# Performance work log

Measured on AMD Instinct MI355X. Metric: run time of the kernel, lower is better.

Reference implementation:

```python
import jax, jax.numpy as jnp
import numpy as np

FEATURE_DIM, HIDDEN_DIM, ATTN_DIM = 2048, 1024, 1024
B, L = 128, 196


def setup_inputs() -> dict:
    key = jax.random.key(0)
    ks = jax.random.split(key, 8)
    s_enc = 1.0 / np.sqrt(FEATURE_DIM)
    s_hid = 1.0 / np.sqrt(HIDDEN_DIM)
    s_full = 1.0 / np.sqrt(ATTN_DIM)
    return {
        "encoder_out": jax.random.normal(ks[0], (B, L, FEATURE_DIM), jnp.float32),
        "hidden": jax.random.normal(ks[1], (B, HIDDEN_DIM), jnp.float32),
        "W_enc": jax.random.uniform(ks[2], (FEATURE_DIM, ATTN_DIM), jnp.float32, -s_enc, s_enc),
        "b_enc": jax.random.uniform(ks[3], (ATTN_DIM,), jnp.float32, -s_enc, s_enc),
        "W_hid": jax.random.uniform(ks[4], (HIDDEN_DIM, ATTN_DIM), jnp.float32, -s_hid, s_hid),
        "b_hid": jax.random.uniform(ks[5], (ATTN_DIM,), jnp.float32, -s_hid, s_hid),
        "W_full": jax.random.uniform(ks[6], (ATTN_DIM,), jnp.float32, -s_full, s_full),
        "b_full": jax.random.uniform(ks[7], (1,), jnp.float32, -s_full, s_full),
    }


def reference(encoder_out, hidden, W_enc, b_enc, W_hid, b_hid, W_full, b_full):
    # attn1: (B, L, A)
    attn1 = jnp.einsum("blf,fa->bla", encoder_out, W_enc) + b_enc
    # attn2: (B, 1, A)
    attn2 = (hidden @ W_hid + b_hid)[:, None, :]
    attn = jax.nn.relu(attn1 + attn2)
    # scalar score per location: (B, L)
    scores = jnp.einsum("bla,a->bl", attn, W_full) + b_full[0]
    alpha = jax.nn.softmax(scores, axis=1)
    # weighted sum over L: (B, F)
    context = jnp.einsum("blf,bl->bf", encoder_out, alpha)
    return context, alpha
```

## Files before the change

### kernel.cpp

```cpp
#include <hip/hip_runtime.h>
#include <hip/hip_bf16.h>

typedef unsigned short u16;
typedef short s16x8 __attribute__((ext_vector_type(8)));
typedef float f32x4 __attribute__((ext_vector_type(4)));

#define F_DIM 2048
#define A_DIM 1024
#define H_DIM 1024
#define BATCH 128
#define LLEN  196
#define MROWS (BATCH * LLEN)
#define LDA   40

__device__ __forceinline__ u16 f2b(float x) {
  union { float f; unsigned int u; } c; c.f = x;
  unsigned int r = (c.u + 0x7fffu + ((c.u >> 16) & 1u)) >> 16;
  return (u16)r;
}

__device__ __forceinline__ void gload_lds16(const void* g, void* l) {
  __builtin_amdgcn_global_load_lds((const __attribute__((address_space(1))) void*)g,
                                   (__attribute__((address_space(3))) void*)l, 16, 0, 0);
}

__global__ void wenc_cvt_kernel(const float* __restrict__ W, u16* __restrict__ WT) {
  __shared__ float tile[32][33];
  int kb = blockIdx.x * 32, ab = blockIdx.y * 32;
  int t = threadIdx.x;
  int r = t >> 3, c = (t & 7) * 4;
  float4 v = *(const float4*)&W[(size_t)(kb + r) * A_DIM + ab + c];
  tile[r][c] = v.x; tile[r][c + 1] = v.y; tile[r][c + 2] = v.z; tile[r][c + 3] = v.w;
  __syncthreads();
  ushort4 o;
  o.x = f2b(tile[c + 0][r]);
  o.y = f2b(tile[c + 1][r]);
  o.z = f2b(tile[c + 2][r]);
  o.w = f2b(tile[c + 3][r]);
  *(ushort4*)&WT[(size_t)(ab + r) * F_DIM + kb + c] = o;
}

__global__ void enc_cvt_kernel(const float* __restrict__ enc, u16* __restrict__ encb) {
  int idx = blockIdx.x * 256 + threadIdx.x;
  const float4* src = (const float4*)enc;
  uint4* dst = (uint4*)encb;
  #pragma unroll
  for (int it = 0; it < 8; ++it) {
    size_t p = (size_t)idx + (size_t)it * 802816;
    float4 v0 = src[p * 2], v1 = src[p * 2 + 1];
    union { u16 u[8]; uint4 q; } o;
    o.u[0] = f2b(v0.x); o.u[1] = f2b(v0.y); o.u[2] = f2b(v0.z); o.u[3] = f2b(v0.w);
    o.u[4] = f2b(v1.x); o.u[5] = f2b(v1.y); o.u[6] = f2b(v1.z); o.u[7] = f2b(v1.w);
    dst[p] = o.q;
  }
}

__global__ void attn2_kernel(const float* __restrict__ hidden, const float* __restrict__ W_hid,
                             const float* __restrict__ b_hid, const float* __restrict__ b_enc,
                             float* __restrict__ attn2p) {
  __shared__ float hl[8][256];
  int t = threadIdx.x;
  int a  = blockIdx.x * 256 + t;
  int b0 = blockIdx.y * 8;
  int k0 = blockIdx.z * 256;
  {
    int j = t >> 5, kk = (t & 31) * 8;
    float4 v0 = *(const float4*)&hidden[(size_t)(b0 + j) * H_DIM + k0 + kk];
    float4 v1 = *(const float4*)&hidden[(size_t)(b0 + j) * H_DIM + k0 + kk + 4];
    hl[j][kk + 0] = v0.x; hl[j][kk + 1] = v0.y; hl[j][kk + 2] = v0.z; hl[j][kk + 3] = v0.w;
    hl[j][kk + 4] = v1.x; hl[j][kk + 5] = v1.y; hl[j][kk + 6] = v1.z; hl[j][kk + 7] = v1.w;
  }
  __syncthreads();
  float acc[8] = {0.f, 0.f, 0.f, 0.f, 0.f, 0.f, 0.f, 0.f};
  #pragma unroll 4
  for (int k = 0; k < 256; ++k) {
    float w = W_hid[(size_t)(k0 + k) * A_DIM + a];
    #pragma unroll
    for (int j = 0; j < 8; ++j) acc[j] = fmaf(hl[j][k], w, acc[j]);
  }
  if (blockIdx.z == 0) {
    float bias = b_hid[a] + b_enc[a];
    #pragma unroll
    for (int j = 0; j < 8; ++j) acc[j] += bias;
  }
  #pragma unroll
  for (int j = 0; j < 8; ++j) atomicAdd(&attn2p[(size_t)(b0 + j) * A_DIM + a], acc[j]);
}

__global__ void gemm_score_bf16(const u16* __restrict__ encb, const u16* __restrict__ WT,
                                const float* __restrict__ attn2p, const float* __restrict__ W_full,
                                float* __restrict__ scores) {
  __shared__ __align__(16) u16 As[128 * 32];
  __shared__ __align__(16) u16 Bs[128 * 32];
  __shared__ float wf_lds[128];
  __shared__ float at2_lds[2][128];

  int n0 = blockIdx.x * 128;
  int m0 = blockIdx.y * 128;
  int t = threadIdx.x;

  int b0 = m0 / LLEN;
  int bnd = (b0 + 1) * LLEN;
  int b1 = min(b0 + 1, BATCH - 1);

  if (t < 128) {
    wf_lds[t] = W_full[n0 + t];
    at2_lds[0][t] = attn2p[(size_t)b0 * A_DIM + n0 + t];
    at2_lds[1][t] = attn2p[(size_t)b1 * A_DIM + n0 + t];
  }

  int lane = t & 63, wave = t >> 6;
  int wr = wave >> 1, wc = wave & 1;
  int c16 = lane & 15, quad = lane >> 4;

  f32x4 acc[4][4];
  #pragma unroll
  for (int i = 0; i < 4; ++i)
    #pragma unroll
    for (int j = 0; j < 4; ++j) acc[i][j] = (f32x4){0.f, 0.f, 0.f, 0.f};

  const u16* agp0 = encb + (size_t)(m0 + (t >> 2)) * F_DIM + (t & 3) * 8;
  const u16* agp1 = agp0 + (size_t)64 * F_DIM;
  const u16* bgp0 = WT + (size_t)(n0 + (t >> 2)) * F_DIM + (t & 3) * 8;
  const u16* bgp1 = bgp0 + (size_t)64 * F_DIM;
  u16* al = As + wave * 512;
  u16* bl = Bs + wave * 512;

  for (int kt = 0; kt < F_DIM; kt += 32) {
    gload_lds16(agp0 + kt, al);
    gload_lds16(agp1 + kt, al + 2048);
    gload_lds16(bgp0 + kt, bl);
    gload_lds16(bgp1 + kt, bl + 2048);
    __syncthreads();
    s16x8 af[4], bf[4];
    #pragma unroll
    for (int i = 0; i < 4; ++i) {
      af[i] = *(const s16x8*)&As[(wr * 64 + i * 16 + c16) * 32 + quad * 8];
      bf[i] = *(const s16x8*)&Bs[(wc * 64 + i * 16 + c16) * 32 + quad * 8];
    }
    #pragma unroll
    for (int mi = 0; mi < 4; ++mi)
      #pragma unroll
      for (int ni = 0; ni < 4; ++ni)
        acc[mi][ni] = __builtin_amdgcn_mfma_f32_16x16x32_bf16(af[mi], bf[ni], acc[mi][ni], 0, 0, 0);
    __syncthreads();
  }

  float wf[4], a2a[4], a2b[4];
  #pragma unroll
  for (int ni = 0; ni < 4; ++ni) {
    int col = wc * 64 + ni * 16 + c16;
    wf[ni] = wf_lds[col];
    a2a[ni] = at2_lds[0][col];
    a2b[ni] = at2_lds[1][col];
  }
  #pragma unroll
  for (int mi = 0; mi < 4; ++mi) {
    #pragma unroll
    for (int r = 0; r < 4; ++r) {
      int row_g = m0 + wr * 64 + mi * 16 + quad * 4 + r;
      bool hi = row_g >= bnd;
      float p = 0.f;
      #pragma unroll
      for (int ni = 0; ni < 4; ++ni) {
        float v = acc[mi][ni][r] + (hi ? a2b[ni] : a2a[ni]);
        v = fmaxf(v, 0.f);
        p = fmaf(v, wf[ni], p);
      }
      p += __shfl_xor(p, 1);
      p += __shfl_xor(p, 2);
      p += __shfl_xor(p, 4);
      p += __shfl_xor(p, 8);
      if (c16 == 0) atomicAdd(&scores[row_g], p);
    }
  }
}

__global__ void gemm_score_f32(const float* __restrict__ enc, const u16* __restrict__ WT,
                               const float* __restrict__ attn2p, const float* __restrict__ W_full,
                               float* __restrict__ scores) {
  __shared__ __align__(16) u16 As[128 * LDA];
  __shared__ __align__(16) u16 Bs[128 * LDA];
  __shared__ float wf_lds[128];
  __shared__ float at2_lds[2][128];

  int n0 = blockIdx.x * 128;
  int m0 = blockIdx.y * 128;
  int t = threadIdx.x;
  int b0 = m0 / LLEN;
  int bnd = (b0 + 1) * LLEN;
  int b1 = min(b0 + 1, BATCH - 1);
  if (t < 128) {
    wf_lds[t] = W_full[n0 + t];
    at2_lds[0][t] = attn2p[(size_t)b0 * A_DIM + n0 + t];
    at2_lds[1][t] = attn2p[(size_t)b1 * A_DIM + n0 + t];
  }
  int lane = t & 63, wave = t >> 6;
  int wr = wave >> 1, wc = wave & 1;
  int c16 = lane & 15, quad = lane >> 4;
  f32x4 acc[4][4];
  #pragma unroll
  for (int i = 0; i < 4; ++i)
    #pragma unroll
    for (int j = 0; j < 4; ++j) acc[i][j] = (f32x4){0.f, 0.f, 0.f, 0.f};
  int ar = t >> 3, ac = (t & 7) * 4;
  int br = t >> 2, bc = (t & 3) * 8;
  const float* ap = enc + (size_t)(m0 + ar) * F_DIM + ac;
  const u16*  bp = WT + (size_t)(n0 + br) * F_DIM + bc;
  for (int kt = 0; kt < F_DIM; kt += 32) {
    #pragma unroll
    for (int p = 0; p < 4; ++p) {
      float4 v = *(const float4*)(ap + (size_t)p * 32 * F_DIM + kt);
      ushort4 u;
      u.x = f2b(v.x); u.y = f2b(v.y); u.z = f2b(v.z); u.w = f2b(v.w);
      *(ushort4*)&As[(ar + p * 32) * LDA + ac] = u;
    }
    #pragma unroll
    for (int p = 0; p < 2; ++p) {
      uint4 v = *(const uint4*)(bp + (size_t)p * 64 * F_DIM + kt);
      *(uint4*)&Bs[(br + p * 64) * LDA + bc] = v;
    }
    __syncthreads();
    s16x8 af[4], bf[4];
    #pragma unroll
    for (int i = 0; i < 4; ++i) {
      af[i] = *(const s16x8*)&As[(wr * 64 + i * 16 + c16) * LDA + quad * 8];
      bf[i] = *(const s16x8*)&Bs[(wc * 64 + i * 16 + c16) * LDA + quad * 8];
    }
    #pragma unroll
    for (int mi = 0; mi < 4; ++mi)
      #pragma unroll
      for (int ni = 0; ni < 4; ++ni)
        acc[mi][ni] = __builtin_amdgcn_mfma_f32_16x16x32_bf16(af[mi], bf[ni], acc[mi][ni], 0, 0, 0);
    __syncthreads();
  }
  float wf[4], a2a[4], a2b[4];
  #pragma unroll
  for (int ni = 0; ni < 4; ++ni) {
    int col = wc * 64 + ni * 16 + c16;
    wf[ni] = wf_lds[col];
    a2a[ni] = at2_lds[0][col];
    a2b[ni] = at2_lds[1][col];
  }
  #pragma unroll
  for (int mi = 0; mi < 4; ++mi) {
    #pragma unroll
    for (int r = 0; r < 4; ++r) {
      int row_g = m0 + wr * 64 + mi * 16 + quad * 4 + r;
      bool hi = row_g >= bnd;
      float p = 0.f;
      #pragma unroll
      for (int ni = 0; ni < 4; ++ni) {
        float v = acc[mi][ni][r] + (hi ? a2b[ni] : a2a[ni]);
        v = fmaxf(v, 0.f);
        p = fmaf(v, wf[ni], p);
      }
      p += __shfl_xor(p, 1);
      p += __shfl_xor(p, 2);
      p += __shfl_xor(p, 4);
      p += __shfl_xor(p, 8);
      if (c16 == 0) atomicAdd(&scores[row_g], p);
    }
  }
}

__global__ void softmax_kernel(const float* __restrict__ scores, float* __restrict__ alpha) {
  __shared__ float red[8];
  int b = blockIdx.x, t = threadIdx.x;
  float s = (t < LLEN) ? scores[b * LLEN + t] : -3.0e38f;
  float m = s;
  #pragma unroll
  for (int o = 1; o <= 32; o <<= 1) m = fmaxf(m, __shfl_xor(m, o));
  if ((t & 63) == 0) red[t >> 6] = m;
  __syncthreads();
  m = fmaxf(fmaxf(red[0], red[1]), fmaxf(red[2], red[3]));
  float e = (t < LLEN) ? expf(s - m) : 0.f;
  float sum = e;
  #pragma unroll
  for (int o = 1; o <= 32; o <<= 1) sum += __shfl_xor(sum, o);
  __syncthreads();
  if ((t & 63) == 0) red[4 + (t >> 6)] = sum;
  __syncthreads();
  sum = red[4] + red[5] + red[6] + red[7];
  if (t < LLEN) alpha[b * LLEN + t] = e / sum;
}

__global__ void context_kernel(const float* __restrict__ enc, const float* __restrict__ alpha,
                               float* __restrict__ out) {
  __shared__ float al[49];
  int b = blockIdx.y, t = threadIdx.x;
  int l0 = blockIdx.z * 49;
  int f4 = blockIdx.x * 256 + t;
  if (t < 49) al[t] = alpha[b * LLEN + l0 + t];
  __syncthreads();
  const float4* e4 = (const float4*)enc + ((size_t)b * LLEN + l0) * (F_DIM / 4) + f4;
  float4 acc = {0.f, 0.f, 0.f, 0.f};
  #pragma unroll 7
  for (int l = 0; l < 49; ++l) {
    float4 v = e4[(size_t)l * (F_DIM / 4)];
    float a = al[l];
    acc.x = fmaf(v.x, a, acc.x);
    acc.y = fmaf(v.y, a, acc.y);
    acc.z = fmaf(v.z, a, acc.z);
    acc.w = fmaf(v.w, a, acc.w);
  }
  float* o = out + (size_t)b * F_DIM + f4 * 4;
  atomicAdd(o + 0, acc.x);
  atomicAdd(o + 1, acc.y);
  atomicAdd(o + 2, acc.z);
  atomicAdd(o + 3, acc.w);
}

extern "C" void kernel_launch(void* const* d_in, const int* in_sizes, int n_in,
                              void* d_out, int out_size, void* d_ws, size_t ws_size,
                              hipStream_t stream) {
  const float* enc    = (const float*)d_in[0];
  const float* hidden = (const float*)d_in[1];
  const float* W_enc  = (const float*)d_in[2];
  const float* b_enc  = (const float*)d_in[3];
  const float* W_hid  = (const float*)d_in[4];
  const float* b_hid  = (const float*)d_in[5];
  const float* W_full = (const float*)d_in[6];
  float* out = (float*)d_out;
  float* alpha_out = out + (size_t)BATCH * F_DIM;

  const size_t encb_bytes = (size_t)MROWS * F_DIM * sizeof(u16);
  const size_t wt_bytes   = (size_t)A_DIM * F_DIM * sizeof(u16);
  const size_t a2_bytes   = (size_t)BATCH * A_DIM * sizeof(float);
  const size_t sc_bytes   = (size_t)MROWS * sizeof(float);
  char* ws = (char*)d_ws;

  if (ws_size >= encb_bytes + wt_bytes + a2_bytes + sc_bytes) {
    u16*   encb   = (u16*)ws;
    u16*   WT     = (u16*)(ws + encb_bytes);
    float* attn2p = (float*)(ws + encb_bytes + wt_bytes);
    float* scores = (float*)(ws + encb_bytes + wt_bytes + a2_bytes);

    hipMemsetAsync(attn2p, 0, a2_bytes, stream);
    hipMemsetAsync(scores, 0, sc_bytes, stream);
    hipMemsetAsync(out, 0, (size_t)BATCH * F_DIM * sizeof(float), stream);

    wenc_cvt_kernel<<<dim3(F_DIM / 32, A_DIM / 32), 256, 0, stream>>>(W_enc, WT);
    enc_cvt_kernel<<<dim3(3136), 256, 0, stream>>>(enc, encb);
    attn2_kernel<<<dim3(A_DIM / 256, BATCH / 8, 4), 256, 0, stream>>>(hidden, W_hid, b_hid, b_enc, attn2p);
    gemm_score_bf16<<<dim3(A_DIM / 128, MROWS / 128), 256, 0, stream>>>(encb, WT, attn2p, W_full, scores);
    softmax_kernel<<<dim3(BATCH), 256, 0, stream>>>(scores, alpha_out);
    context_kernel<<<dim3(F_DIM / 4 / 256, BATCH, 4), 256, 0, stream>>>(enc, alpha_out, out);
  } else {
    u16*   WT     = (u16*)ws;
    float* attn2p = (float*)(ws + wt_bytes);
    float* scores = (float*)(ws + wt_bytes + a2_bytes);

    hipMemsetAsync(attn2p, 0, a2_bytes, stream);
    hipMemsetAsync(scores, 0, sc_bytes, stream);
    hipMemsetAsync(out, 0, (size_t)BATCH * F_DIM * sizeof(float), stream);

    wenc_cvt_kernel<<<dim3(F_DIM / 32, A_DIM / 32), 256, 0, stream>>>(W_enc, WT);
    attn2_kernel<<<dim3(A_DIM / 256, BATCH / 8, 4), 256, 0, stream>>>(hidden, W_hid, b_hid, b_enc, attn2p);
    gemm_score_f32<<<dim3(A_DIM / 128, MROWS / 128), 256, 0, stream>>>(enc, WT, attn2p, W_full, scores);
    softmax_kernel<<<dim3(BATCH), 256, 0, stream>>>(scores, alpha_out);
    context_kernel<<<dim3(F_DIM / 4 / 256, BATCH, 4), 256, 0, stream>>>(enc, alpha_out, out);
  }
}
```

Baseline: 534.4 us.

## Swizzle GEMM tile order for L2 reuse and compute context from bf16 encoder

The bf16 GEMM now runs on a 1D grid remapped so that groups of 8 M-tiles sweep all N-tiles together, which is meant to keep A and B tiles resident in L2 and cut DRAM re-reads. The context reduction now reads the bf16 copy of the encoder output instead of the fp32 original, halving the bytes streamed. That kernel uses fewer, larger blocks with 28 rows each. The cost is reduced precision in the context output, since encoder values are bf16-rounded, and more atomics into the output.

```diff
diff --git a/kernel.cpp b/kernel.cpp
--- a/kernel.cpp
+++ b/kernel.cpp
@@ -17,6 +17,11 @@
   union { float f; unsigned int u; } c; c.f = x;
   unsigned int r = (c.u + 0x7fffu + ((c.u >> 16) & 1u)) >> 16;
   return (u16)r;
+}
+
+__device__ __forceinline__ float b2f(u16 x) {
+  union { unsigned int u; float f; } c; c.u = ((unsigned int)x) << 16;
+  return c.f;
 }
 
 __device__ __forceinline__ void gload_lds16(const void* g, void* l) {
@@ -95,8 +100,16 @@
   __shared__ float wf_lds[128];
   __shared__ float at2_lds[2][128];
 
-  int n0 = blockIdx.x * 128;
-  int m0 = blockIdx.y * 128;
+  int i = blockIdx.x;
+  int g  = i >> 6;
+  int r  = i & 63;
+  int y  = r >> 3;
+  int gi = r & 7;
+  int mt = g * 8 + gi;
+  if (mt >= MROWS / 128) return;
+
+  int n0 = y * 128;
+  int m0 = mt * 128;
   int t = threadIdx.x;
 
   int b0 = m0 / LLEN;
@@ -115,9 +128,9 @@
 
   f32x4 acc[4][4];
   #pragma unroll
-  for (int i = 0; i < 4; ++i)
-    #pragma unroll
-    for (int j = 0; j < 4; ++j) acc[i][j] = (f32x4){0.f, 0.f, 0.f, 0.f};
+  for (int ii = 0; ii < 4; ++ii)
+    #pragma unroll
+    for (int j = 0; j < 4; ++j) acc[ii][j] = (f32x4){0.f, 0.f, 0.f, 0.f};
 
   const u16* agp0 = encb + (size_t)(m0 + (t >> 2)) * F_DIM + (t & 3) * 8;
   const u16* agp1 = agp0 + (size_t)64 * F_DIM;
@@ -134,9 +147,9 @@
     __syncthreads();
     s16x8 af[4], bf[4];
     #pragma unroll
-    for (int i = 0; i < 4; ++i) {
-      af[i] = *(const s16x8*)&As[(wr * 64 + i * 16 + c16) * 32 + quad * 8];
-      bf[i] = *(const s16x8*)&Bs[(wc * 64 + i * 16 + c16) * 32 + quad * 8];
+    for (int ii = 0; ii < 4; ++ii) {
+      af[ii] = *(const s16x8*)&As[(wr * 64 + ii * 16 + c16) * 32 + quad * 8];
+      bf[ii] = *(const s16x8*)&Bs[(wc * 64 + ii * 16 + c16) * 32 + quad * 8];
     }
     #pragma unroll
     for (int mi = 0; mi < 4; ++mi)
@@ -146,6 +159,94 @@
     __syncthreads();
   }
 
+  float wf[4], a2a[4], a2b[4];
+  #pragma unroll
+  for (int ni = 0; ni < 4; ++ni) {
+    int col = wc * 64 + ni * 16 + c16;
+    wf[ni] = wf_lds[col];
+    a2a[ni] = at2_lds[0][col];
+    a2b[ni] = at2_lds[1][col];
+  }
+  #pragma unroll
+  for (int mi = 0; mi < 4; ++mi) {
+    #pragma unroll
+    for (int rr = 0; rr < 4; ++rr) {
+      int row_g = m0 + wr * 64 + mi * 16 + quad * 4 + rr;
+      bool hi = row_g >= bnd;
+      float p = 0.f;
+      #pragma unroll
+      for (int ni = 0; ni < 4; ++ni) {
+        float v = acc[mi][ni][rr] + (hi ? a2b[ni] : a2a[ni]);
+        v = fmaxf(v, 0.f);
+        p = fmaf(v, wf[ni], p);
+      }
+      p += __shfl_xor(p, 1);
+      p += __shfl_xor(p, 2);
+      p += __shfl_xor(p, 4);
+      p += __shfl_xor(p, 8);
+      if (c16 == 0) atomicAdd(&scores[row_g], p);
+    }
+  }
+}
+
+__global__ void gemm_score_f32(const float* __restrict__ enc, const u16* __restrict__ WT,
+                               const float* __restrict__ attn2p, const float* __restrict__ W_full,
+                               float* __restrict__ scores) {
+  __shared__ __align__(16) u16 As[128 * LDA];
+  __shared__ __align__(16) u16 Bs[128 * LDA];
+  __shared__ float wf_lds[128];
+  __shared__ float at2_lds[2][128];
+
+  int n0 = blockIdx.x * 128;
+  int m0 = blockIdx.y * 128;
+  int t = threadIdx.x;
+  int b0 = m0 / LLEN;
+  int bnd = (b0 + 1) * LLEN;
+  int b1 = min(b0 + 1, BATCH - 1);
+  if (t < 128) {
+    wf_lds[t] = W_full[n0 + t];
+    at2_lds[0][t] = attn2p[(size_t)b0 * A_DIM + n0 + t];
+    at2_lds[1][t] = attn2p[(size_t)b1 * A_DIM + n0 + t];
+  }
+  int lane = t & 63, wave = t >> 6;
+  int wr = wave >> 1, wc = wave & 1;
+  int c16 = lane & 15, quad = lane >> 4;
+  f32x4 acc[4][4];
+  #pragma unroll
+  for (int i = 0; i < 4; ++i)
+    #pragma unroll
+    for (int j = 0; j < 4; ++j) acc[i][j] = (f32x4){0.f, 0.f, 0.f, 0.f};
+  int ar = t >> 3, ac = (t & 7) * 4;
+  int br = t >> 2, bc = (t & 3) * 8;
+  const float* ap = enc + (size_t)(m0 + ar) * F_DIM + ac;
+  const u16*  bp = WT + (size_t)(n0 + br) * F_DIM + bc;
+  for (int kt = 0; kt < F_DIM; kt += 32) {
+    #pragma unroll
+    for (int p = 0; p < 4; ++p) {
+      float4 v = *(const float4*)(ap + (size_t)p * 32 * F_DIM + kt);
+      ushort4 u;
+      u.x = f2b(v.x); u.y = f2b(v.y); u.z = f2b(v.z); u.w = f2b(v.w);
+      *(ushort4*)&As[(ar + p * 32) * LDA + ac] = u;
+    }
+    #pragma unroll
+    for (int p = 0; p < 2; ++p) {
+      uint4 v = *(const uint4*)(bp + (size_t)p * 64 * F_DIM + kt);
+      *(uint4*)&Bs[(br + p * 64) * LDA + bc] = v;
+    }
+    __syncthreads();
+    s16x8 af[4], bf[4];
+    #pragma unroll
+    for (int i = 0; i < 4; ++i) {
+      af[i] = *(const s16x8*)&As[(wr * 64 + i * 16 + c16) * LDA + quad * 8];
+      bf[i] = *(const s16x8*)&Bs[(wc * 64 + i * 16 + c16) * LDA + quad * 8];
+    }
+    #pragma unroll
+    for (int mi = 0; mi < 4; ++mi)
+      #pragma unroll
+      for (int ni = 0; ni < 4; ++ni)
+        acc[mi][ni] = __builtin_amdgcn_mfma_f32_16x16x32_bf16(af[mi], bf[ni], acc[mi][ni], 0, 0, 0);
+    __syncthreads();
+  }
   float wf[4], a2a[4], a2b[4];
   #pragma unroll
   for (int ni = 0; ni < 4; ++ni) {
@@ -176,94 +277,6 @@
   }
 }
 
-__global__ void gemm_score_f32(const float* __restrict__ enc, const u16* __restrict__ WT,
-                               const float* __restrict__ attn2p, const float* __restrict__ W_full,
-                               float* __restrict__ scores) {
-  __shared__ __align__(16) u16 As[128 * LDA];
-  __shared__ __align__(16) u16 Bs[128 * LDA];
-  __shared__ float wf_lds[128];
-  __shared__ float at2_lds[2][128];
-
-  int n0 = blockIdx.x * 128;
-  int m0 = blockIdx.y * 128;
-  int t = threadIdx.x;
-  int b0 = m0 / LLEN;
-  int bnd = (b0 + 1) * LLEN;
-  int b1 = min(b0 + 1, BATCH - 1);
-  if (t < 128) {
-    wf_lds[t] = W_full[n0 + t];
-    at2_lds[0][t] = attn2p[(size_t)b0 * A_DIM + n0 + t];
-    at2_lds[1][t] = attn2p[(size_t)b1 * A_DIM + n0 + t];
-  }
-  int lane = t & 63, wave = t >> 6;
-  int wr = wave >> 1, wc = wave & 1;
-  int c16 = lane & 15, quad = lane >> 4;
-  f32x4 acc[4][4];
-  #pragma unroll
-  for (int i = 0; i < 4; ++i)
-    #pragma unroll
-    for (int j = 0; j < 4; ++j) acc[i][j] = (f32x4){0.f, 0.f, 0.f, 0.f};
-  int ar = t >> 3, ac = (t & 7) * 4;
-  int br = t >> 2, bc = (t & 3) * 8;
-  const float* ap = enc + (size_t)(m0 + ar) * F_DIM + ac;
-  const u16*  bp = WT + (size_t)(n0 + br) * F_DIM + bc;
-  for (int kt = 0; kt < F_DIM; kt += 32) {
-    #pragma unroll
-    for (int p = 0; p < 4; ++p) {
-      float4 v = *(const float4*)(ap + (size_t)p * 32 * F_DIM + kt);
-      ushort4 u;
-      u.x = f2b(v.x); u.y = f2b(v.y); u.z = f2b(v.z); u.w = f2b(v.w);
-      *(ushort4*)&As[(ar + p * 32) * LDA + ac] = u;
-    }
-    #pragma unroll
-    for (int p = 0; p < 2; ++p) {
-      uint4 v = *(const uint4*)(bp + (size_t)p * 64 * F_DIM + kt);
-      *(uint4*)&Bs[(br + p * 64) * LDA + bc] = v;
-    }
-    __syncthreads();
-    s16x8 af[4], bf[4];
-    #pragma unroll
-    for (int i = 0; i < 4; ++i) {
-      af[i] = *(const s16x8*)&As[(wr * 64 + i * 16 + c16) * LDA + quad * 8];
-      bf[i] = *(const s16x8*)&Bs[(wc * 64 + i * 16 + c16) * LDA + quad * 8];
-    }
-    #pragma unroll
-    for (int mi = 0; mi < 4; ++mi)
-      #pragma unroll
-      for (int ni = 0; ni < 4; ++ni)
-        acc[mi][ni] = __builtin_amdgcn_mfma_f32_16x16x32_bf16(af[mi], bf[ni], acc[mi][ni], 0, 0, 0);
-    __syncthreads();
-  }
-  float wf[4], a2a[4], a2b[4];
-  #pragma unroll
-  for (int ni = 0; ni < 4; ++ni) {
-    int col = wc * 64 + ni * 16 + c16;
-    wf[ni] = wf_lds[col];
-    a2a[ni] = at2_lds[0][col];
-    a2b[ni] = at2_lds[1][col];
-  }
-  #pragma unroll
-  for (int mi = 0; mi < 4; ++mi) {
-    #pragma unroll
-    for (int r = 0; r < 4; ++r) {
-      int row_g = m0 + wr * 64 + mi * 16 + quad * 4 + r;
-      bool hi = row_g >= bnd;
-      float p = 0.f;
-      #pragma unroll
-      for (int ni = 0; ni < 4; ++ni) {
-        float v = acc[mi][ni][r] + (hi ? a2b[ni] : a2a[ni]);
-        v = fmaxf(v, 0.f);
-        p = fmaf(v, wf[ni], p);
-      }
-      p += __shfl_xor(p, 1);
-      p += __shfl_xor(p, 2);
-      p += __shfl_xor(p, 4);
-      p += __shfl_xor(p, 8);
-      if (c16 == 0) atomicAdd(&scores[row_g], p);
-    }
-  }
-}
-
 __global__ void softmax_kernel(const float* __restrict__ scores, float* __restrict__ alpha) {
   __shared__ float red[8];
   int b = blockIdx.x, t = threadIdx.x;
@@ -283,6 +296,28 @@
   __syncthreads();
   sum = red[4] + red[5] + red[6] + red[7];
   if (t < LLEN) alpha[b * LLEN + t] = e / sum;
+}
+
+__global__ void context_bf16_kernel(const u16* __restrict__ encb, const float* __restrict__ alpha,
+                                    float* __restrict__ out) {
+  __shared__ float al[28];
+  int b = blockIdx.y, t = threadIdx.x;
+  int l0 = blockIdx.x * 28;
+  if (t < 28) al[t] = alpha[b * LLEN + l0 + t];
+  __syncthreads();
+  const uint4* e4 = (const uint4*)(encb + ((size_t)b * LLEN + l0) * F_DIM) + t;
+  float acc[8] = {0.f, 0.f, 0.f, 0.f, 0.f, 0.f, 0.f, 0.f};
+  #pragma unroll 4
+  for (int l = 0; l < 28; ++l) {
+    uint4 v = e4[(size_t)l * (F_DIM / 8)];
+    float a = al[l];
+    const u16* u = (const u16*)&v;
+    #pragma unroll
+    for (int j = 0; j < 8; ++j) acc[j] = fmaf(b2f(u[j]), a, acc[j]);
+  }
+  float* o = out + (size_t)b * F_DIM + t * 8;
+  #pragma unroll
+  for (int j = 0; j < 8; ++j) atomicAdd(o + j, acc[j]);
 }
 
 __global__ void context_kernel(const float* __restrict__ enc, const float* __restrict__ alpha,
@@ -343,9 +378,9 @@
     wenc_cvt_kernel<<<dim3(F_DIM / 32, A_DIM / 32), 256, 0, stream>>>(W_enc, WT);
     enc_cvt_kernel<<<dim3(3136), 256, 0, stream>>>(enc, encb);
     attn2_kernel<<<dim3(A_DIM / 256, BATCH / 8, 4), 256, 0, stream>>>(hidden, W_hid, b_hid, b_enc, attn2p);
-    gemm_score_bf16<<<dim3(A_DIM / 128, MROWS / 128), 256, 0, stream>>>(encb, WT, attn2p, W_full, scores);
+    gemm_score_bf16<<<dim3(1600), 256, 0, stream>>>(encb, WT, attn2p, W_full, scores);
     softmax_kernel<<<dim3(BATCH), 256, 0, stream>>>(scores, alpha_out);
-    context_kernel<<<dim3(F_DIM / 4 / 256, BATCH, 4), 256, 0, stream>>>(enc, alpha_out, out);
+    context_bf16_kernel<<<dim3(7, BATCH), 256, 0, stream>>>(encb, alpha_out, out);
   } else {
     u16*   WT     = (u16*)ws;
     float* attn2p = (float*)(ws + wt_bytes);
```

Result: no change. 540.0 us (+1.0%).
